# Performance work log

Hardware: AMD Instinct MI355X
Metric: run time of the kernel (lower is better)

## Reference

```python
import jax, jax.numpy as jnp
import numpy as np

N = 50000
E = 800000
IN_DIM = 128
HID = 32
HEADS = 4
OUT_DIM = 32
NEG_SLOPE = 0.2


def setup_inputs() -> dict:
    key = jax.random.key(0)
    ks = jax.random.split(key, 10)
    x = jax.random.normal(ks[0], (N, IN_DIM), dtype=jnp.float32)
    edge_index = jax.random.randint(ks[1], (2, E), 0, N, dtype=jnp.int64)
    # layer 1: in 128 -> 4 heads x 32, concat
    W1 = jax.random.normal(ks[2], (IN_DIM, HEADS * HID), dtype=jnp.float32) * (1.0 / np.sqrt(IN_DIM))
    a_src1 = jax.random.normal(ks[3], (HEADS, HID), dtype=jnp.float32) * 0.1
    a_dst1 = jax.random.normal(ks[4], (HEADS, HID), dtype=jnp.float32) * 0.1
    b1 = jnp.zeros((HEADS * HID,), dtype=jnp.float32)
    # layer 2: in 128 -> 1 head x 32, mean
    W2 = jax.random.normal(ks[5], (HEADS * HID, OUT_DIM), dtype=jnp.float32) * (1.0 / np.sqrt(HEADS * HID))
    a_src2 = jax.random.normal(ks[6], (1, OUT_DIM), dtype=jnp.float32) * 0.1
    a_dst2 = jax.random.normal(ks[7], (1, OUT_DIM), dtype=jnp.float32) * 0.1
    b2 = jnp.zeros((OUT_DIM,), dtype=jnp.float32)
    return {"x": x, "edge_index": edge_index, "W1": W1, "a_src1": a_src1,
            "a_dst1": a_dst1, "b1": b1, "W2": W2, "a_src2": a_src2,
            "a_dst2": a_dst2, "b2": b2}


def gat_layer(x, src, dst, W, a_src, a_dst, b, heads, concat, num_nodes):
    # linear transform -> [N, H, C]
    h = (x @ W).reshape(num_nodes, heads, -1)
    # per-node attention halves, gathered per edge -> [E, H]
    alpha = jax.nn.leaky_relu((h * a_src).sum(-1)[src] + (h * a_dst).sum(-1)[dst],
                              negative_slope=NEG_SLOPE)
    # segment softmax over edges grouped by destination node
    seg_max = jax.ops.segment_max(alpha, dst, num_segments=num_nodes)
    e = jnp.exp(alpha - seg_max[dst])
    denom = jax.ops.segment_sum(e, dst, num_segments=num_nodes)[dst]
    w = e / jnp.maximum(denom, 1e-16)
    # weighted message scatter-sum -> [N, H, C]
    out = jax.ops.segment_sum(h[src] * w[..., None], dst, num_segments=num_nodes)
    out = out.reshape(num_nodes, -1) if concat else out.mean(axis=1)
    return out + b


def reference(x, edge_index, W1, a_src1, a_dst1, b1, W2, a_src2, a_dst2, b2):
    num_nodes = x.shape[0]
    loops = jnp.arange(num_nodes, dtype=edge_index.dtype)
    src = jnp.concatenate([edge_index[0], loops])  # add self-loops (PyG default)
    dst = jnp.concatenate([edge_index[1], loops])
    h = jax.nn.relu(gat_layer(x, src, dst, W1, a_src1, a_dst1, b1, HEADS, True, num_nodes))
    out = gat_layer(h, src, dst, W2, a_src2, a_dst2, b2, 1, False, num_nodes)
    return jax.nn.sigmoid(out)
```

## Files before the change

kernel.cpp:

```cpp
#include <hip/hip_runtime.h>
#include <math.h>

#define NN 50000
#define NE 800000
#define NT (NN + NE)
#define SCAN_BLOCKS 196

__device__ __forceinline__ float lrelu(float a) { return a > 0.f ? a : 0.2f * a; }

__device__ __forceinline__ float sel4(float4 v, int h) {
  float r = v.x;
  r = (h == 1) ? v.y : r;
  r = (h == 2) ? v.z : r;
  r = (h == 3) ? v.w : r;
  return r;
}

__device__ __forceinline__ unsigned int f2bf(float f) {
  unsigned int u = __float_as_uint(f);
  return (u + 0x7FFFu + ((u >> 16) & 1u)) >> 16;
}
__device__ __forceinline__ unsigned int packbf(float lo, float hi) {
  return f2bf(lo) | (f2bf(hi) << 16);
}
__device__ __forceinline__ float bflo(unsigned int v) { return __uint_as_float(v << 16); }
__device__ __forceinline__ float bfhi(unsigned int v) { return __uint_as_float(v & 0xFFFF0000u); }

__global__ void k_detect(const unsigned int* __restrict__ eb, int* __restrict__ flag) {
  __shared__ int nz;
  if (threadIdx.x == 0) nz = 0;
  __syncthreads();
  int local = 0;
  for (int i = threadIdx.x; i < 2048; i += 256) local |= (eb[2 * i + 1] != 0u);
  if (local) nz = 1;
  __syncthreads();
  if (threadIdx.x == 0) *flag = (nz == 0) ? 1 : 0;
}

__global__ __launch_bounds__(256) void k_pass1(const void* __restrict__ eb,
                                               const int* __restrict__ flag,
                                               int* __restrict__ cnt,
                                               unsigned int* __restrict__ pw) {
  int e0 = (blockIdx.x * 256 + threadIdx.x) * 4;
  if (e0 >= NT) return;
  int is64 = *flag;
  int d0, d1, d2, d3;
  if (e0 < NE) {
    if (is64) {
      const uint4* p = (const uint4*)((const unsigned int*)eb + 2 * ((size_t)NE + e0));
      uint4 a = p[0], b = p[1];
      d0 = (int)a.x; d1 = (int)a.z; d2 = (int)b.x; d3 = (int)b.z;
    } else {
      int4 v = *(const int4*)((const int*)eb + (size_t)NE + e0);
      d0 = v.x; d1 = v.y; d2 = v.z; d3 = v.w;
    }
  } else {
    d0 = e0 - NE; d1 = d0 + 1; d2 = d0 + 2; d3 = d0 + 3;
  }
  unsigned int p0 = (unsigned int)atomicAdd(&cnt[d0], 1);
  unsigned int p1 = (unsigned int)atomicAdd(&cnt[d1], 1);
  unsigned int p2 = (unsigned int)atomicAdd(&cnt[d2], 1);
  unsigned int p3 = (unsigned int)atomicAdd(&cnt[d3], 1);
  *(uint4*)&pw[e0] = make_uint4(p0, p1, p2, p3);
}

__global__ __launch_bounds__(256) void k_bsum(const int* __restrict__ cnt,
                                              int* __restrict__ bsum) {
  int i = blockIdx.x * 256 + threadIdx.x;
  int v = (i < NN) ? cnt[i] : 0;
#pragma unroll
  for (int off = 1; off < 64; off <<= 1) v += __shfl_xor(v, off, 64);
  __shared__ int ws[4];
  int lane = threadIdx.x & 63, wid = threadIdx.x >> 6;
  if (lane == 0) ws[wid] = v;
  __syncthreads();
  if (threadIdx.x == 0) bsum[blockIdx.x] = ws[0] + ws[1] + ws[2] + ws[3];
}

__global__ __launch_bounds__(256) void k_bscan(const int* __restrict__ bsum,
                                               int* __restrict__ boff,
                                               int* __restrict__ rowp) {
  int t = threadIdx.x;
  int lane = t & 63, wid = t >> 6;
  int v = (t < SCAN_BLOCKS) ? bsum[t] : 0;
  int incl = v;
#pragma unroll
  for (int off = 1; off < 64; off <<= 1) {
    int u = __shfl_up(incl, off, 64);
    if (lane >= off) incl += u;
  }
  __shared__ int wsum[4], woff[4];
  if (lane == 63) wsum[wid] = incl;
  __syncthreads();
  if (t == 0) {
    woff[0] = 0;
    woff[1] = wsum[0];
    woff[2] = wsum[0] + wsum[1];
    woff[3] = wsum[0] + wsum[1] + wsum[2];
  }
  __syncthreads();
  if (t < SCAN_BLOCKS) boff[t] = woff[wid] + incl - v;
  if (t == 0) rowp[NN] = NT;
}

__global__ __launch_bounds__(256) void k_rowp(const int* __restrict__ cnt,
                                              const int* __restrict__ boff,
                                              int* __restrict__ rowp) {
  int i = blockIdx.x * 256 + threadIdx.x;
  int t = threadIdx.x;
  int lane = t & 63, wid = t >> 6;
  int v = (i < NN) ? cnt[i] : 0;
  int incl = v;
#pragma unroll
  for (int off = 1; off < 64; off <<= 1) {
    int u = __shfl_up(incl, off, 64);
    if (lane >= off) incl += u;
  }
  __shared__ int wsum[4], woff[4];
  if (lane == 63) wsum[wid] = incl;
  __syncthreads();
  if (t == 0) {
    woff[0] = 0;
    woff[1] = wsum[0];
    woff[2] = wsum[0] + wsum[1];
    woff[3] = wsum[0] + wsum[1] + wsum[2];
  }
  __syncthreads();
  if (i < NN) rowp[i] = boff[blockIdx.x] + woff[wid] + incl - v;
}

__global__ __launch_bounds__(256) void k_pass2(const void* __restrict__ eb,
                                               const int* __restrict__ flag,
                                               const int* __restrict__ rowp,
                                               const unsigned int* __restrict__ pw,
                                               int* __restrict__ csr) {
  int e0 = (blockIdx.x * 256 + threadIdx.x) * 4;
  if (e0 >= NT) return;
  int is64 = *flag;
  int s0, s1, s2, s3, d0, d1, d2, d3;
  if (e0 < NE) {
    if (is64) {
      const uint4* ps = (const uint4*)((const unsigned int*)eb + 2 * (size_t)e0);
      uint4 a = ps[0], b = ps[1];
      s0 = (int)a.x; s1 = (int)a.z; s2 = (int)b.x; s3 = (int)b.z;
      const uint4* pd = (const uint4*)((const unsigned int*)eb + 2 * ((size_t)NE + e0));
      uint4 c = pd[0], d = pd[1];
      d0 = (int)c.x; d1 = (int)c.z; d2 = (int)d.x; d3 = (int)d.z;
    } else {
      int4 vs = *(const int4*)((const int*)eb + (size_t)e0);
      s0 = vs.x; s1 = vs.y; s2 = vs.z; s3 = vs.w;
      int4 vd = *(const int4*)((const int*)eb + (size_t)NE + e0);
      d0 = vd.x; d1 = vd.y; d2 = vd.z; d3 = vd.w;
    }
  } else {
    s0 = d0 = e0 - NE;
    s1 = d1 = d0 + 1;
    s2 = d2 = d0 + 2;
    s3 = d3 = d0 + 3;
  }
  uint4 pv = *(const uint4*)&pw[e0];
  csr[rowp[d0] + (int)pv.x] = s0;
  csr[rowp[d1] + (int)pv.y] = s1;
  csr[rowp[d2] + (int)pv.z] = s2;
  csr[rowp[d3] + (int)pv.w] = s3;
}

__global__ __launch_bounds__(256) void k_gemm1(const float* __restrict__ X,
                                               const float* __restrict__ W,
                                               const float* __restrict__ a_src,
                                               const float* __restrict__ a_dst,
                                               uint2* __restrict__ Hb,
                                               float* __restrict__ AS,
                                               float* __restrict__ AD) {
  __shared__ float xt[32 * 132];
  __shared__ float wt[32 * 132];
  int tid = threadIdx.x;
  int tr = tid >> 4, tc = tid & 15;
  int r0 = blockIdx.x * 128;
  float acc[8][8];
#pragma unroll
  for (int i = 0; i < 8; ++i)
#pragma unroll
    for (int j = 0; j < 8; ++j) acc[i][j] = 0.f;

  for (int kb = 0; kb < 4; ++kb) {
    __syncthreads();
#pragma unroll
    for (int i = tid; i < 1024; i += 256) {
      int row = i >> 3, k4 = i & 7;
      int gr = r0 + row;
      float4 v = make_float4(0.f, 0.f, 0.f, 0.f);
      if (gr < NN) v = ((const float4*)X)[(size_t)gr * 32 + kb * 8 + k4];
      xt[(k4 * 4 + 0) * 132 + row] = v.x;
      xt[(k4 * 4 + 1) * 132 + row] = v.y;
      xt[(k4 * 4 + 2) * 132 + row] = v.z;
      xt[(k4 * 4 + 3) * 132 + row] = v.w;
    }
#pragma unroll
    for (int i = tid; i < 1024; i += 256) {
      int kr = i >> 5, c4 = i & 31;
      *(float4*)&wt[kr * 132 + c4 * 4] = ((const float4*)W)[(size_t)(kb * 32 + kr) * 32 + c4];
    }
    __syncthreads();
#pragma unroll 2
    for (int k = 0; k < 32; ++k) {
      float4 xa = *(const float4*)&xt[k * 132 + tr * 8];
      float4 xb = *(const float4*)&xt[k * 132 + tr * 8 + 4];
      float4 wa = *(const float4*)&wt[k * 132 + tc * 4];
      float4 wb = *(const float4*)&wt[k * 132 + tc * 4 + 64];
      float xr[8] = {xa.x, xa.y, xa.z, xa.w, xb.x, xb.y, xb.z, xb.w};
      float wc[8] = {wa.x, wa.y, wa.z, wa.w, wb.x, wb.y, wb.z, wb.w};
#pragma unroll
      for (int i = 0; i < 8; ++i)
#pragma unroll
        for (int j = 0; j < 8; ++j) acc[i][j] += xr[i] * wc[j];
    }
  }
  float4 sA = ((const float4*)a_src)[tc];
  float4 sB = ((const float4*)a_src)[16 + tc];
  float4 dA = ((const float4*)a_dst)[tc];
  float4 dB = ((const float4*)a_dst)[16 + tc];
#pragma unroll
  for (int i = 0; i < 8; ++i) {
    int gr = r0 + tr * 8 + i;
    float psA = acc[i][0] * sA.x + acc[i][1] * sA.y + acc[i][2] * sA.z + acc[i][3] * sA.w;
    float psB = acc[i][4] * sB.x + acc[i][5] * sB.y + acc[i][6] * sB.z + acc[i][7] * sB.w;
    float pdA = acc[i][0] * dA.x + acc[i][1] * dA.y + acc[i][2] * dA.z + acc[i][3] * dA.w;
    float pdB = acc[i][4] * dB.x + acc[i][5] * dB.y + acc[i][6] * dB.z + acc[i][7] * dB.w;
#pragma unroll
    for (int off = 1; off < 8; off <<= 1) {
      psA += __shfl_xor(psA, off, 64);
      psB += __shfl_xor(psB, off, 64);
      pdA += __shfl_xor(pdA, off, 64);
      pdB += __shfl_xor(pdB, off, 64);
    }
    if (gr < NN) {
      Hb[(size_t)gr * 32 + tc] = make_uint2(packbf(acc[i][0], acc[i][1]),
                                            packbf(acc[i][2], acc[i][3]));
      Hb[(size_t)gr * 32 + 16 + tc] = make_uint2(packbf(acc[i][4], acc[i][5]),
                                                 packbf(acc[i][6], acc[i][7]));
      if (tc == 0) {
        AS[gr * 4 + 0] = psA; AS[gr * 4 + 2] = psB;
        AD[gr * 4 + 0] = pdA; AD[gr * 4 + 2] = pdB;
      } else if (tc == 8) {
        AS[gr * 4 + 1] = psA; AS[gr * 4 + 3] = psB;
        AD[gr * 4 + 1] = pdA; AD[gr * 4 + 3] = pdB;
      }
    }
  }
}

__global__ __launch_bounds__(256) void k_l1node(const int* __restrict__ rowp,
                                                const int* __restrict__ csr,
                                                const uint4* __restrict__ Hb,
                                                const float* __restrict__ AS,
                                                const float* __restrict__ AD,
                                                const float* __restrict__ b1,
                                                uint4* __restrict__ HMb) {
  int lane = threadIdx.x & 63, wid = threadIdx.x >> 6;
  int n = blockIdx.x * 4 + wid;
  if (n >= NN) return;
  int beg = rowp[n], end = rowp[n + 1];
  float4 ad4 = *(const float4*)&AD[n * 4];

  int sl = lane & 15;
  int g = lane >> 4;
  int hd = sl >> 2;
  float adh = sel4(ad4, hd);

  float a0 = 0.f, a1 = 0.f, a2 = 0.f, a3 = 0.f, a4 = 0.f, a5 = 0.f, a6 = 0.f, a7 = 0.f;
  float esum = 0.f;
  int i = beg + g;
  for (; i + 4 < end; i += 8) {
    int sA = csr[i];
    int sB = csr[i + 4];
    float lA = AS[sA * 4 + hd];
    float lB = AS[sB * 4 + hd];
    uint4 hA = Hb[(size_t)sA * 16 + sl];
    uint4 hB = Hb[(size_t)sB * 16 + sl];
    float wA = __expf(lrelu(lA + adh));
    float wB = __expf(lrelu(lB + adh));
    esum += wA + wB;
    a0 += wA * bflo(hA.x) + wB * bflo(hB.x);
    a1 += wA * bfhi(hA.x) + wB * bfhi(hB.x);
    a2 += wA * bflo(hA.y) + wB * bflo(hB.y);
    a3 += wA * bfhi(hA.y) + wB * bfhi(hB.y);
    a4 += wA * bflo(hA.z) + wB * bflo(hB.z);
    a5 += wA * bfhi(hA.z) + wB * bfhi(hB.z);
    a6 += wA * bflo(hA.w) + wB * bflo(hB.w);
    a7 += wA * bfhi(hA.w) + wB * bfhi(hB.w);
  }
  if (i < end) {
    int s = csr[i];
    float l = AS[s * 4 + hd];
    uint4 hv = Hb[(size_t)s * 16 + sl];
    float w0 = __expf(lrelu(l + adh));
    esum += w0;
    a0 += w0 * bflo(hv.x);
    a1 += w0 * bfhi(hv.x);
    a2 += w0 * bflo(hv.y);
    a3 += w0 * bfhi(hv.y);
    a4 += w0 * bflo(hv.z);
    a5 += w0 * bfhi(hv.z);
    a6 += w0 * bflo(hv.w);
    a7 += w0 * bfhi(hv.w);
  }
#pragma unroll
  for (int off = 16; off < 64; off <<= 1) {
    esum += __shfl_xor(esum, off, 64);
    a0 += __shfl_xor(a0, off, 64);
    a1 += __shfl_xor(a1, off, 64);
    a2 += __shfl_xor(a2, off, 64);
    a3 += __shfl_xor(a3, off, 64);
    a4 += __shfl_xor(a4, off, 64);
    a5 += __shfl_xor(a5, off, 64);
    a6 += __shfl_xor(a6, off, 64);
    a7 += __shfl_xor(a7, off, 64);
  }
  if (lane < 16) {
    float r = 1.f / esum;
    int c = sl * 8;
    float4 bva = *(const float4*)&b1[c];
    float4 bvb = *(const float4*)&b1[c + 4];
    float v0 = fmaxf(a0 * r + bva.x, 0.f);
    float v1 = fmaxf(a1 * r + bva.y, 0.f);
    float v2 = fmaxf(a2 * r + bva.z, 0.f);
    float v3 = fmaxf(a3 * r + bva.w, 0.f);
    float v4 = fmaxf(a4 * r + bvb.x, 0.f);
    float v5 = fmaxf(a5 * r + bvb.y, 0.f);
    float v6 = fmaxf(a6 * r + bvb.z, 0.f);
    float v7 = fmaxf(a7 * r + bvb.w, 0.f);
    HMb[(size_t)n * 16 + sl] =
        make_uint4(packbf(v0, v1), packbf(v2, v3), packbf(v4, v5), packbf(v6, v7));
  }
}

__global__ __launch_bounds__(256) void k_gemm2(const uint4* __restrict__ HMb,
                                               const float* __restrict__ W2,
                                               const float* __restrict__ a_src2,
                                               const float* __restrict__ a_dst2,
                                               uint4* __restrict__ Hb2,
                                               float* __restrict__ AS,
                                               float* __restrict__ AD) {
  __shared__ float wsm[128 * 32];
  int tid = threadIdx.x;
  for (int i = tid; i < 1024; i += 256) ((float4*)wsm)[i] = ((const float4*)W2)[i];
  __syncthreads();
  int rl = tid >> 2, sub = tid & 3;
  int r = blockIdx.x * 64 + rl;
  float acc[32];
#pragma unroll
  for (int j = 0; j < 32; ++j) acc[j] = 0.f;

  if (r < NN) {
    const uint4* xp = &HMb[(size_t)r * 16 + sub * 4];
    uint4 xq0 = xp[0], xq1 = xp[1], xq2 = xp[2], xq3 = xp[3];
    int kbase = sub * 32;
    unsigned int wds[16] = {xq0.x, xq0.y, xq0.z, xq0.w, xq1.x, xq1.y, xq1.z, xq1.w,
                            xq2.x, xq2.y, xq2.z, xq2.w, xq3.x, xq3.y, xq3.z, xq3.w};
#pragma unroll
    for (int t = 0; t < 16; ++t) {
      float xlo = bflo(wds[t]);
      float xhi = bfhi(wds[t]);
      const float4* wr0 = (const float4*)&wsm[(kbase + t * 2) * 32];
      const float4* wr1 = (const float4*)&wsm[(kbase + t * 2 + 1) * 32];
#pragma unroll
      for (int j4 = 0; j4 < 8; ++j4) {
        float4 w0 = wr0[j4];
        float4 w1 = wr1[j4];
        acc[j4 * 4 + 0] += xlo * w0.x + xhi * w1.x;
        acc[j4 * 4 + 1] += xlo * w0.y + xhi * w1.y;
        acc[j4 * 4 + 2] += xlo * w0.z + xhi * w1.z;
        acc[j4 * 4 + 3] += xlo * w0.w + xhi * w1.w;
      }
    }
  }
#pragma unroll
  for (int j = 0; j < 32; ++j) {
    acc[j] += __shfl_xor(acc[j], 1, 64);
    acc[j] += __shfl_xor(acc[j], 2, 64);
  }
  if (r < NN) {
    int c = sub * 8;
    float4 sv0 = ((const float4*)a_src2)[sub * 2];
    float4 sv1 = ((const float4*)a_src2)[sub * 2 + 1];
    float4 dv0 = ((const float4*)a_dst2)[sub * 2];
    float4 dv1 = ((const float4*)a_dst2)[sub * 2 + 1];
    float ps = acc[c + 0] * sv0.x + acc[c + 1] * sv0.y + acc[c + 2] * sv0.z +
               acc[c + 3] * sv0.w + acc[c + 4] * sv1.x + acc[c + 5] * sv1.y +
               acc[c + 6] * sv1.z + acc[c + 7] * sv1.w;
    float pd = acc[c + 0] * dv0.x + acc[c + 1] * dv0.y + acc[c + 2] * dv0.z +
               acc[c + 3] * dv0.w + acc[c + 4] * dv1.x + acc[c + 5] * dv1.y +
               acc[c + 6] * dv1.z + acc[c + 7] * dv1.w;
    ps += __shfl_xor(ps, 1, 64);
    ps += __shfl_xor(ps, 2, 64);
    pd += __shfl_xor(pd, 1, 64);
    pd += __shfl_xor(pd, 2, 64);
    Hb2[(size_t)r * 4 + sub] =
        make_uint4(packbf(acc[c + 0], acc[c + 1]), packbf(acc[c + 2], acc[c + 3]),
                   packbf(acc[c + 4], acc[c + 5]), packbf(acc[c + 6], acc[c + 7]));
    if (sub == 0) {
      AS[r] = ps;
      AD[r] = pd;
    }
  }
}

__global__ __launch_bounds__(256) void k_l2node(const int* __restrict__ rowp,
                                                const int* __restrict__ csr,
                                                const uint2* __restrict__ Hb2,
                                                const float* __restrict__ AS,
                                                const float* __restrict__ AD,
                                                const float* __restrict__ b2,
                                                float* __restrict__ out) {
  int lane = threadIdx.x & 63, wid = threadIdx.x >> 6;
  int n = blockIdx.x * 4 + wid;
  if (n >= NN) return;
  int beg = rowp[n], end = rowp[n + 1];
  float adn = AD[n];

  int sl = lane & 7;
  int g = lane >> 3;
  float a0 = 0.f, a1 = 0.f, a2 = 0.f, a3 = 0.f;
  float esum = 0.f;
  int i = beg + g;
  for (; i + 8 < end; i += 16) {
    int sA = csr[i];
    int sB = csr[i + 8];
    float lA = AS[sA];
    float lB = AS[sB];
    uint2 hA = Hb2[(size_t)sA * 8 + sl];
    uint2 hB = Hb2[(size_t)sB * 8 + sl];
    float wA = __expf(lrelu(lA + adn));
    float wB = __expf(lrelu(lB + adn));
    esum += wA + wB;
    a0 += wA * bflo(hA.x) + wB * bflo(hB.x);
    a1 += wA * bfhi(hA.x) + wB * bfhi(hB.x);
    a2 += wA * bflo(hA.y) + wB * bflo(hB.y);
    a3 += wA * bfhi(hA.y) + wB * bfhi(hB.y);
  }
  if (i < end) {
    int s = csr[i];
    float l = AS[s];
    uint2 hv = Hb2[(size_t)s * 8 + sl];
    float w0 = __expf(lrelu(l + adn));
    esum += w0;
    a0 += w0 * bflo(hv.x);
    a1 += w0 * bfhi(hv.x);
    a2 += w0 * bflo(hv.y);
    a3 += w0 * bfhi(hv.y);
  }
#pragma unroll
  for (int off = 8; off < 64; off <<= 1) {
    esum += __shfl_xor(esum, off, 64);
    a0 += __shfl_xor(a0, off, 64);
    a1 += __shfl_xor(a1, off, 64);
    a2 += __shfl_xor(a2, off, 64);
    a3 += __shfl_xor(a3, off, 64);
  }
  if (lane < 8) {
    float r = 1.f / esum;
    int c = sl * 4;
    float4 bv = *(const float4*)&b2[c];
    float vx = a0 * r + bv.x, vy = a1 * r + bv.y, vz = a2 * r + bv.z, vw = a3 * r + bv.w;
    *(float4*)&out[(size_t)n * 32 + c] =
        make_float4(1.f / (1.f + __expf(-vx)), 1.f / (1.f + __expf(-vy)),
                    1.f / (1.f + __expf(-vz)), 1.f / (1.f + __expf(-vw)));
  }
}

extern "C" void kernel_launch(void* const* d_in, const int* in_sizes, int n_in,
                              void* d_out, int out_size, void* d_ws, size_t ws_size,
                              hipStream_t stream) {
  (void)in_sizes; (void)n_in; (void)out_size; (void)ws_size;
  const float* x      = (const float*)d_in[0];
  const void*  eb     = d_in[1];
  const float* W1     = (const float*)d_in[2];
  const float* a_src1 = (const float*)d_in[3];
  const float* a_dst1 = (const float*)d_in[4];
  const float* b1     = (const float*)d_in[5];
  const float* W2     = (const float*)d_in[6];
  const float* a_src2 = (const float*)d_in[7];
  const float* a_dst2 = (const float*)d_in[8];
  const float* b2     = (const float*)d_in[9];
  float* out = (float*)d_out;

  char* w = (char*)d_ws;
  auto alloc = [&](size_t bytes) {
    char* p = w;
    w += (bytes + 255) & ~(size_t)255;
    return p;
  };
  int*          flag = (int*)alloc(4);
  int*          cnt  = (int*)alloc((size_t)NN * 4);
  int*          rowp = (int*)alloc((size_t)(NN + 1) * 4);
  unsigned int* pw   = (unsigned int*)alloc((size_t)NT * 4);
  int*          csr  = (int*)alloc((size_t)NT * 4);
  int*          bsum = (int*)alloc((size_t)SCAN_BLOCKS * 4);
  int*          boff = (int*)alloc((size_t)SCAN_BLOCKS * 4);
  uint4*        Hb1  = (uint4*)alloc((size_t)NN * 128 * 2);
  float*        AS1  = (float*)alloc((size_t)NN * 16);
  float*        AD1  = (float*)alloc((size_t)NN * 16);
  uint4*        HMb  = (uint4*)alloc((size_t)NN * 128 * 2);
  uint4* Hb2 = Hb1;
  float* AS2 = (float*)cnt;
  float* AD2 = (float*)pw;

  hipMemsetAsync(cnt, 0, (size_t)NN * 4, stream);
  k_detect<<<1, 256, 0, stream>>>((const unsigned int*)eb, flag);
  int egrid4 = (NT / 4 + 255) / 256;
  k_pass1<<<egrid4, 256, 0, stream>>>(eb, flag, cnt, pw);
  k_bsum<<<SCAN_BLOCKS, 256, 0, stream>>>(cnt, bsum);
  k_bscan<<<1, 256, 0, stream>>>(bsum, boff, rowp);
  k_rowp<<<SCAN_BLOCKS, 256, 0, stream>>>(cnt, boff, rowp);
  k_pass2<<<egrid4, 256, 0, stream>>>(eb, flag, rowp, pw, csr);

  k_gemm1<<<(NN + 127) / 128, 256, 0, stream>>>(x, W1, a_src1, a_dst1, (uint2*)Hb1, AS1, AD1);
  k_l1node<<<(NN + 3) / 4, 256, 0, stream>>>(rowp, csr, Hb1, AS1, AD1, b1, HMb);
  k_gemm2<<<(NN + 63) / 64, 256, 0, stream>>>(HMb, W2, a_src2, a_dst2, Hb2, AS2, AD2);
  k_l2node<<<(NN + 3) / 4, 256, 0, stream>>>(rowp, csr, (const uint2*)Hb2, AS2, AD2, b2, out);
}
```

Measured before the change: 278.3 us.

## Shrink gemm1 tile to 32 rows with 8x2 per-thread outputs for more blocks

Reworks the first-layer GEMM from 128-row tiles with an 8x8 register block per thread to 32-row tiles where each thread computes 8 rows by 2 adjacent columns. Each 16-lane group now covers one head, so the attention dot-product reduction becomes a 16-lane shuffle and one store per head. The change raises block count about fourfold and cuts register pressure, improving occupancy and wave-level parallelism. In exchange each block reloads the full W tile for fewer rows, there is less register reuse per shared-memory load, and there are more shuffles.

```diff
diff --git a/kernel.cpp b/kernel.cpp
--- a/kernel.cpp
+++ b/kernel.cpp
@@ -169,32 +169,32 @@
                                                const float* __restrict__ W,
                                                const float* __restrict__ a_src,
                                                const float* __restrict__ a_dst,
-                                               uint2* __restrict__ Hb,
+                                               unsigned int* __restrict__ Hb,
                                                float* __restrict__ AS,
                                                float* __restrict__ AD) {
-  __shared__ float xt[32 * 132];
+  __shared__ float xt[32 * 36];
   __shared__ float wt[32 * 132];
   int tid = threadIdx.x;
-  int tr = tid >> 4, tc = tid & 15;
-  int r0 = blockIdx.x * 128;
-  float acc[8][8];
-#pragma unroll
-  for (int i = 0; i < 8; ++i)
-#pragma unroll
-    for (int j = 0; j < 8; ++j) acc[i][j] = 0.f;
+  int tr = tid >> 6, tc = tid & 63;
+  int r0 = blockIdx.x * 32;
+  float acc[8][2];
+#pragma unroll
+  for (int i = 0; i < 8; ++i) {
+    acc[i][0] = 0.f;
+    acc[i][1] = 0.f;
+  }
 
   for (int kb = 0; kb < 4; ++kb) {
     __syncthreads();
-#pragma unroll
-    for (int i = tid; i < 1024; i += 256) {
-      int row = i >> 3, k4 = i & 7;
+    {
+      int row = tid >> 3, k4 = tid & 7;
       int gr = r0 + row;
       float4 v = make_float4(0.f, 0.f, 0.f, 0.f);
       if (gr < NN) v = ((const float4*)X)[(size_t)gr * 32 + kb * 8 + k4];
-      xt[(k4 * 4 + 0) * 132 + row] = v.x;
-      xt[(k4 * 4 + 1) * 132 + row] = v.y;
-      xt[(k4 * 4 + 2) * 132 + row] = v.z;
-      xt[(k4 * 4 + 3) * 132 + row] = v.w;
+      xt[(k4 * 4 + 0) * 36 + row] = v.x;
+      xt[(k4 * 4 + 1) * 36 + row] = v.y;
+      xt[(k4 * 4 + 2) * 36 + row] = v.z;
+      xt[(k4 * 4 + 3) * 36 + row] = v.w;
     }
 #pragma unroll
     for (int i = tid; i < 1024; i += 256) {
@@ -202,49 +202,37 @@
       *(float4*)&wt[kr * 132 + c4 * 4] = ((const float4*)W)[(size_t)(kb * 32 + kr) * 32 + c4];
     }
     __syncthreads();
-#pragma unroll 2
+#pragma unroll 4
     for (int k = 0; k < 32; ++k) {
-      float4 xa = *(const float4*)&xt[k * 132 + tr * 8];
-      float4 xb = *(const float4*)&xt[k * 132 + tr * 8 + 4];
-      float4 wa = *(const float4*)&wt[k * 132 + tc * 4];
-      float4 wb = *(const float4*)&wt[k * 132 + tc * 4 + 64];
+      float4 xa = *(const float4*)&xt[k * 36 + tr * 8];
+      float4 xb = *(const float4*)&xt[k * 36 + tr * 8 + 4];
+      float2 wv = *(const float2*)&wt[k * 132 + tc * 2];
       float xr[8] = {xa.x, xa.y, xa.z, xa.w, xb.x, xb.y, xb.z, xb.w};
-      float wc[8] = {wa.x, wa.y, wa.z, wa.w, wb.x, wb.y, wb.z, wb.w};
-#pragma unroll
-      for (int i = 0; i < 8; ++i)
-#pragma unroll
-        for (int j = 0; j < 8; ++j) acc[i][j] += xr[i] * wc[j];
-    }
-  }
-  float4 sA = ((const float4*)a_src)[tc];
-  float4 sB = ((const float4*)a_src)[16 + tc];
-  float4 dA = ((const float4*)a_dst)[tc];
-  float4 dB = ((const float4*)a_dst)[16 + tc];
+#pragma unroll
+      for (int i = 0; i < 8; ++i) {
+        acc[i][0] += xr[i] * wv.x;
+        acc[i][1] += xr[i] * wv.y;
+      }
+    }
+  }
+  int head = tc >> 4;
+  float2 sv = *(const float2*)&a_src[tc * 2];
+  float2 dv = *(const float2*)&a_dst[tc * 2];
 #pragma unroll
   for (int i = 0; i < 8; ++i) {
     int gr = r0 + tr * 8 + i;
-    float psA = acc[i][0] * sA.x + acc[i][1] * sA.y + acc[i][2] * sA.z + acc[i][3] * sA.w;
-    float psB = acc[i][4] * sB.x + acc[i][5] * sB.y + acc[i][6] * sB.z + acc[i][7] * sB.w;
-    float pdA = acc[i][0] * dA.x + acc[i][1] * dA.y + acc[i][2] * dA.z + acc[i][3] * dA.w;
-    float pdB = acc[i][4] * dB.x + acc[i][5] * dB.y + acc[i][6] * dB.z + acc[i][7] * dB.w;
-#pragma unroll
-    for (int off = 1; off < 8; off <<= 1) {
-      psA += __shfl_xor(psA, off, 64);
-      psB += __shfl_xor(psB, off, 64);
-      pdA += __shfl_xor(pdA, off, 64);
-      pdB += __shfl_xor(pdB, off, 64);
+    float ps = acc[i][0] * sv.x + acc[i][1] * sv.y;
+    float pd = acc[i][0] * dv.x + acc[i][1] * dv.y;
+#pragma unroll
+    for (int off = 1; off < 16; off <<= 1) {
+      ps += __shfl_xor(ps, off, 64);
+      pd += __shfl_xor(pd, off, 64);
     }
     if (gr < NN) {
-      Hb[(size_t)gr * 32 + tc] = make_uint2(packbf(acc[i][0], acc[i][1]),
-                                            packbf(acc[i][2], acc[i][3]));
-      Hb[(size_t)gr * 32 + 16 + tc] = make_uint2(packbf(acc[i][4], acc[i][5]),
-                                                 packbf(acc[i][6], acc[i][7]));
-      if (tc == 0) {
-        AS[gr * 4 + 0] = psA; AS[gr * 4 + 2] = psB;
-        AD[gr * 4 + 0] = pdA; AD[gr * 4 + 2] = pdB;
-      } else if (tc == 8) {
-        AS[gr * 4 + 1] = psA; AS[gr * 4 + 3] = psB;
-        AD[gr * 4 + 1] = pdA; AD[gr * 4 + 3] = pdB;
+      Hb[(size_t)gr * 64 + tc] = packbf(acc[i][0], acc[i][1]);
+      if ((tc & 15) == 0) {
+        AS[gr * 4 + head] = ps;
+        AD[gr * 4 + head] = pd;
       }
     }
   }
@@ -515,7 +503,8 @@
   k_rowp<<<SCAN_BLOCKS, 256, 0, stream>>>(cnt, boff, rowp);
   k_pass2<<<egrid4, 256, 0, stream>>>(eb, flag, rowp, pw, csr);
 
-  k_gemm1<<<(NN + 127) / 128, 256, 0, stream>>>(x, W1, a_src1, a_dst1, (uint2*)Hb1, AS1, AD1);
+  k_gemm1<<<(NN + 31) / 32, 256, 0, stream>>>(x, W1, a_src1, a_dst1,
+                                              (unsigned int*)Hb1, AS1, AD1);
   k_l1node<<<(NN + 3) / 4, 256, 0, stream>>>(rowp, csr, Hb1, AS1, AD1, b1, HMb);
   k_gemm2<<<(NN + 63) / 64, 256, 0, stream>>>(HMb, W2, a_src2, a_dst2, Hb2, AS2, AD2);
   k_l2node<<<(NN + 3) / 4, 256, 0, stream>>>(rowp, csr, (const uint2*)Hb2, AS2, AD2, b2, out);
```

Result: no change. 275.1 us (-1.1%).
